# Kernel tuning notes

Hardware: AMD Instinct MI355X
Metric: run time of the kernel (lower is better)

## Reference

```python
import jax, jax.numpy as jnp
import numpy as np

B, T, C = 16, 2048, 64  # n_embd = 64


def setup_inputs() -> dict:
    key = jax.random.key(0)
    ks = jax.random.split(key, 4)
    scale = 1.0 / np.sqrt(C)
    x = jax.random.normal(ks[0], (B, T, C), dtype=jnp.float32)
    Wk = jax.random.normal(ks[1], (C, C), dtype=jnp.float32) * scale
    Wq = jax.random.normal(ks[2], (C, C), dtype=jnp.float32) * scale
    Wv = jax.random.normal(ks[3], (C, C), dtype=jnp.float32) * scale
    bk = jnp.zeros((C,), dtype=jnp.float32)
    bq = jnp.zeros((C,), dtype=jnp.float32)
    bv = jnp.zeros((C,), dtype=jnp.float32)
    return {"x": x, "Wk": Wk, "bk": bk, "Wq": Wq, "bq": bq, "Wv": Wv, "bv": bv}


def reference(x, Wk, bk, Wq, bq, Wv, bv):
    # Faithful to source: wei = q @ k^T * C**0.5 (MULTIPLY, as in original code),
    # softmax over last axis, no causal mask (tril is built but unused), dropout=0.
    _, _, c = x.shape
    k = jnp.einsum('btc,cd->btd', x, Wk) + bk
    q = jnp.einsum('btc,cd->btd', x, Wq) + bq
    v = jnp.einsum('btc,cd->btd', x, Wv) + bv
    wei = jnp.einsum('btd,bsd->bts', q, k) * (c ** 0.5)  # [B,T,T]
    wei = jax.nn.softmax(wei, axis=-1)
    out = jnp.einsum('bts,bsd->btd', wei, v)  # [B,T,C]
    return out
```

## Files before the change

### kernel.cpp

```cpp
#include <hip/hip_runtime.h>
#include <hip/hip_bf16.h>
#include <stdint.h>

#define NBATCH 16
#define NT 2048
#define NC 64
#define QT 64
#define KT 128
#define SC_LOG2E 11.5415603f

typedef __bf16 bf16x8 __attribute__((ext_vector_type(8)));
typedef _Float16 f16x8 __attribute__((ext_vector_type(8)));
typedef float f32x4 __attribute__((ext_vector_type(4)));
typedef float f32x16 __attribute__((ext_vector_type(16)));

#define Z16 {0.f,0.f,0.f,0.f,0.f,0.f,0.f,0.f,0.f,0.f,0.f,0.f,0.f,0.f,0.f,0.f}

extern "C" __device__ float __ocml_native_exp2_f32(float);
#define EXP2F(x) __ocml_native_exp2_f32(x)

static __device__ __forceinline__ unsigned short f2bf(float f) {
  __bf16 h = (__bf16)f;
  union { __bf16 h; unsigned short u; } a; a.h = h; return a.u;
}
static __device__ __forceinline__ float bf2f(unsigned short h) {
  union { uint32_t u; float f; } a; a.u = ((uint32_t)h) << 16;
  return a.f;
}
static __device__ __forceinline__ unsigned short f2h(float f) {
  _Float16 h = (_Float16)f;
  union { _Float16 h; unsigned short u; } a; a.h = h; return a.u;
}
static __device__ __forceinline__ float h2f(unsigned short u) {
  union { unsigned short u; _Float16 h; } a; a.u = u; return (float)a.h;
}
static __device__ __forceinline__ float fasu(uint32_t u) {
  union { uint32_t u; float f; } a; a.u = u; return a.f;
}
static __device__ __forceinline__ uint32_t uasf(float f) {
  union { float f; uint32_t u; } a; a.f = f; return a.u;
}
static __device__ __forceinline__ uint32_t pkh(float a, float b) {
  auto h = __builtin_amdgcn_cvt_pkrtz(a, b);
  union { decltype(h) v; uint32_t u; } c; c.v = h; return c.u;
}

#define GLD_LDS16(gsrc, ldst)                                                  \
  __builtin_amdgcn_global_load_lds(                                            \
      (const __attribute__((address_space(1))) void*)(gsrc),                   \
      (__attribute__((address_space(3))) void*)(ldst), 16, 0, 0)

__global__ __launch_bounds__(256, 2) void prep_w(
    const float* __restrict__ Wk, const float* __restrict__ Wq,
    const float* __restrict__ Wv,
    unsigned short* __restrict__ wt_hi, unsigned short* __restrict__ wt_lo)
{
  __shared__ unsigned short hbuf[64][66];
  __shared__ unsigned short lbuf[64][66];
  const int m = (int)blockIdx.x;
  const float* Wm = (m == 0) ? Wk : (m == 1 ? Wq : Wv);
  const int tid = (int)threadIdx.x;
  for (int idx = tid; idx < 1024; idx += 256) {
    int c = idx >> 4, o4 = (idx & 15) * 4;
    float4 v = *(const float4*)(Wm + c * 64 + o4);
    float vals[4] = {v.x, v.y, v.z, v.w};
#pragma unroll
    for (int j = 0; j < 4; ++j) {
      unsigned short h = f2bf(vals[j]);
      hbuf[o4 + j][c] = h;
      lbuf[o4 + j][c] = f2bf(vals[j] - bf2f(h));
    }
  }
  __syncthreads();
  for (int idx = tid; idx < 1024; idx += 256) {
    int o = idx >> 4, c0 = (idx & 15) * 4;
    ushort4 hv, lv;
    hv.x = hbuf[o][c0]; hv.y = hbuf[o][c0 + 1];
    hv.z = hbuf[o][c0 + 2]; hv.w = hbuf[o][c0 + 3];
    lv.x = lbuf[o][c0]; lv.y = lbuf[o][c0 + 1];
    lv.z = lbuf[o][c0 + 2]; lv.w = lbuf[o][c0 + 3];
    *(ushort4*)(wt_hi + (size_t)(m * 64 + o) * 64 + c0) = hv;
    *(ushort4*)(wt_lo + (size_t)(m * 64 + o) * 64 + c0) = lv;
  }
}

__global__ __launch_bounds__(256, 2) void proj_kernel(
    const float* __restrict__ x,
    const unsigned short* __restrict__ wt_hi, const unsigned short* __restrict__ wt_lo,
    const float* __restrict__ bk, const float* __restrict__ bq, const float* __restrict__ bv,
    unsigned short* __restrict__ kf, unsigned short* __restrict__ qfh,
    unsigned short* __restrict__ qfl, unsigned short* __restrict__ vt)
{
  __shared__ __align__(16) char smem[65536];
  const int XH = 0, XL = 8192, WTH = 16384, WTL = 40960, VTB = 0;
  const int tid = (int)threadIdx.x;
  const int l = tid & 63, w = tid >> 6;
  const int lr = l & 15, lg = l >> 4;
  const int blk = (int)blockIdx.x;
  const int rowbase = blk * 64;
  const int bb = blk >> 5;

  float4 xv[4];
#pragma unroll
  for (int j = 0; j < 4; ++j) {
    int c = tid + j * 256;
    int row = c >> 4, d0 = (c & 15) * 4;
    xv[j] = *(const float4*)(x + (size_t)(rowbase + row) * NC + d0);
  }
#pragma unroll
  for (int ch4 = 0; ch4 < 6; ++ch4) {
    int ch = ch4 * 4 + w;
    int d = ch * 1024 + l * 16;
    int swk = d ^ (((d >> 7) & 7) << 4);
    GLD_LDS16((const char*)wt_hi + swk, smem + WTH + ch * 1024);
    GLD_LDS16((const char*)wt_lo + swk, smem + WTL + ch * 1024);
  }
#pragma unroll
  for (int j = 0; j < 4; ++j) {
    int c = tid + j * 256;
    int row = c >> 4, d0 = (c & 15) * 4;
    unsigned short h0 = f2bf(xv[j].x), h1 = f2bf(xv[j].y), h2 = f2bf(xv[j].z), h3 = f2bf(xv[j].w);
    unsigned short m0 = f2bf(xv[j].x - bf2f(h0)), m1 = f2bf(xv[j].y - bf2f(h1));
    unsigned short m2 = f2bf(xv[j].z - bf2f(h2)), m3 = f2bf(xv[j].w - bf2f(h3));
    uint2 ph, pl;
    ph.x = (uint32_t)h0 | ((uint32_t)h1 << 16); ph.y = (uint32_t)h2 | ((uint32_t)h3 << 16);
    pl.x = (uint32_t)m0 | ((uint32_t)m1 << 16); pl.y = (uint32_t)m2 | ((uint32_t)m3 << 16);
    int byteoff = (row * 128 + d0 * 2) ^ ((row & 7) << 4);
    *(uint2*)(smem + XH + byteoff) = ph;
    *(uint2*)(smem + XL + byteoff) = pl;
  }
  __syncthreads();

  bf16x8 xh[2], xl[2];
  {
    int row = w * 16 + lr;
#pragma unroll
    for (int dc = 0; dc < 2; ++dc) {
      int byteoff = (row * 128 + (dc * 32 + lg * 8) * 2) ^ ((row & 7) << 4);
      xh[dc] = *(const bf16x8*)(smem + XH + byteoff);
      xl[dc] = *(const bf16x8*)(smem + XL + byteoff);
    }
  }
  f32x4 acc[12];
#pragma unroll
  for (int nb = 0; nb < 12; ++nb) {
    f32x4 a = {0.f, 0.f, 0.f, 0.f};
    int og = nb * 16 + lr;
#pragma unroll
    for (int dc = 0; dc < 2; ++dc) {
      int byteoff = (og * 128 + (dc * 32 + lg * 8) * 2) ^ ((og & 7) << 4);
      bf16x8 bh = *(const bf16x8*)(smem + WTH + byteoff);
      bf16x8 bl = *(const bf16x8*)(smem + WTL + byteoff);
      a = __builtin_amdgcn_mfma_f32_16x16x32_bf16(bh, xh[dc], a, 0, 0, 0);
      a = __builtin_amdgcn_mfma_f32_16x16x32_bf16(bl, xh[dc], a, 0, 0, 0);
      a = __builtin_amdgcn_mfma_f32_16x16x32_bf16(bh, xl[dc], a, 0, 0, 0);
    }
    acc[nb] = a;
  }
  __syncthreads();

  const int tloc = w * 16 + lr;
  const size_t gt = (size_t)(rowbase + tloc);
#pragma unroll
  for (int nb = 0; nb < 12; ++nb) {
    int ogb = (nb & 3) * 16 + lg * 4;
    const float* bp = (nb < 4) ? bk : (nb < 8 ? bq : bv);
    float4 bias = *(const float4*)(bp + ogb);
    float v0 = acc[nb][0] + bias.x, v1 = acc[nb][1] + bias.y,
          v2 = acc[nb][2] + bias.z, v3 = acc[nb][3] + bias.w;
    if (nb < 4) {
      ushort4 hv;
      hv.x = f2h(v0); hv.y = f2h(v1); hv.z = f2h(v2); hv.w = f2h(v3);
      *(ushort4*)(kf + gt * 64 + ogb) = hv;
    } else if (nb < 8) {
      v0 *= SC_LOG2E; v1 *= SC_LOG2E; v2 *= SC_LOG2E; v3 *= SC_LOG2E;
      ushort4 hv, lv;
      hv.x = f2h(v0); lv.x = f2h(v0 - h2f(hv.x));
      hv.y = f2h(v1); lv.y = f2h(v1 - h2f(hv.y));
      hv.z = f2h(v2); lv.z = f2h(v2 - h2f(hv.z));
      hv.w = f2h(v3); lv.w = f2h(v3 - h2f(hv.w));
      *(ushort4*)(qfh + gt * 64 + ogb) = hv;
      *(ushort4*)(qfl + gt * 64 + ogb) = lv;
    } else {
      float vs[4] = {v0, v1, v2, v3};
#pragma unroll
      for (int r = 0; r < 4; ++r) {
        int o = ogb + r;
        int byteoff = (o * 128 + tloc * 2) ^ ((o & 7) << 4);
        *(unsigned short*)(smem + VTB + byteoff) = f2h(vs[r]);
      }
    }
  }
  __syncthreads();
  for (int cc = tid; cc < 512; cc += 256) {
    int o = cc >> 3, t0 = (cc & 7) * 8;
    int byteoff = (o * 128 + t0 * 2) ^ ((o & 7) << 4);
    uint4 v = *(const uint4*)(smem + VTB + byteoff);
    *(uint4*)(vt + ((size_t)bb * 64 + o) * NT + (size_t)(blk & 31) * 64 + t0) = v;
  }
}

__global__ __launch_bounds__(512, 4) void attn_kernel(
    const unsigned short* __restrict__ kf, const unsigned short* __restrict__ qfh,
    const unsigned short* __restrict__ qfl, const unsigned short* __restrict__ vt,
    float* __restrict__ out)
{
  __shared__ __align__(16) char smem[65536];
  const int KB_A = 0, KB_B = 16384;
  const int VB_0 = 32768, VB_1 = 49152;
  const int MLB = 49152;
  const int tid = (int)threadIdx.x;
  const int l = tid & 63, w = tid >> 6;
  const int lq = l & 31;
  const bool hi = (l >= 32);
  const int hioff = hi ? 16 : 0;
  const int r = w & 1;
  const int cc = w >> 1;
  const int lb = ((int)(blockIdx.x & 7) << 6) | ((int)blockIdx.x >> 3);
  const int bb = lb >> 5;
  const int qt = lb & 31;

  const char* k_base = (const char*)(kf + (size_t)bb * NT * 64);
  const char* v_base = (const char*)(vt + (size_t)bb * 64 * NT);

#define STAGE_TILE(kb_, vb_, it_)                                              \
  do {                                                                         \
    const char* k_t = k_base + (size_t)(it_) * 16384;                          \
    const char* v_tb = v_base + (size_t)(it_) * 256;                           \
    _Pragma("unroll")                                                          \
    for (int j = 0; j < 2; ++j) {                                              \
      int ch = 2 * w + j;                                                      \
      int d = ch * 1024 + l * 16;                                              \
      int swk = d ^ (((d >> 7) & 7) << 4);                                     \
      GLD_LDS16(k_t + swk, smem + (kb_) + ch * 1024);                          \
      int o = d >> 8;                                                          \
      int swv = (d & 255) ^ ((o & 7) << 4);                                    \
      GLD_LDS16(v_tb + (size_t)o * 4096 + swv, smem + (vb_) + ch * 1024);      \
    }                                                                          \
  } while (0)

  STAGE_TILE(KB_A, VB_0, 0);
  f16x8 Qh[4], Ql[4];
  {
    const char* qh_t = (const char*)qfh + ((size_t)bb * NT + (size_t)qt * QT) * 128;
    const char* ql_t = (const char*)qfl + ((size_t)bb * NT + (size_t)qt * QT) * 128;
    int qrow = r * 32 + lq;
#pragma unroll
    for (int dc = 0; dc < 4; ++dc) {
      Qh[dc] = *(const f16x8*)(qh_t + qrow * 128 + dc * 32 + hioff);
      Ql[dc] = *(const f16x8*)(ql_t + qrow * 128 + dc * 32 + hioff);
    }
  }
  asm volatile("s_waitcnt vmcnt(0)" ::: "memory");
  __builtin_amdgcn_s_barrier();
  asm volatile("" ::: "memory");

  f32x16 O0 = Z16, O1 = Z16;
  float mrun = -1e30f, lrun = 0.f;
  const int swr = (lq & 7) << 4;

  for (int it = 0; it < NT / KT; ++it) {
    const int cbk = (it & 1) ? KB_B : KB_A;
    const int cbv = (it & 1) ? VB_1 : VB_0;
    if (it + 1 < NT / KT)
      STAGE_TILE((it & 1) ? KB_A : KB_B, (it & 1) ? VB_0 : VB_1, it + 1);

    f32x16 S = Z16;
    __builtin_amdgcn_s_setprio(1);
#pragma unroll
    for (int dc = 0; dc < 4; ++dc) {
      int krow = cc * 32 + lq;
      int cchunk = (dc * 32 + hioff) ^ swr;
      f16x8 Kf = *(const f16x8*)(smem + cbk + krow * 128 + cchunk);
      S = __builtin_amdgcn_mfma_f32_32x32x16_f16(Kf, Qh[dc], S, 0, 0, 0);
      S = __builtin_amdgcn_mfma_f32_32x32x16_f16(Kf, Ql[dc], S, 0, 0, 0);
    }
    __builtin_amdgcn_s_setprio(0);

    float a01 = fmaxf(S[0], S[1]),   a23 = fmaxf(S[2], S[3]);
    float a45 = fmaxf(S[4], S[5]),   a67 = fmaxf(S[6], S[7]);
    float a89 = fmaxf(S[8], S[9]),   aab = fmaxf(S[10], S[11]);
    float acd = fmaxf(S[12], S[13]), aef = fmaxf(S[14], S[15]);
    float pmax = fmaxf(fmaxf(fmaxf(a01, a23), fmaxf(a45, a67)),
                       fmaxf(fmaxf(a89, aab), fmaxf(acd, aef)));
    {
      auto sw = __builtin_amdgcn_permlane32_swap(uasf(pmax), uasf(pmax), false, false);
      pmax = fmaxf(fasu(sw[0]), fasu(sw[1]));
    }
    if (__any(pmax > mrun + 11.55f)) {
      float mnew = fmaxf(mrun, pmax);
      float alpha = EXP2F(mrun - mnew);
      O0 *= alpha; O1 *= alpha; lrun *= alpha; mrun = mnew;
    }
    float p[16];
    float ts = 0.f;
#pragma unroll
    for (int i = 0; i < 16; ++i) { p[i] = EXP2F(S[i] - mrun); ts += p[i]; }
    {
      auto sw = __builtin_amdgcn_permlane32_swap(uasf(ts), uasf(ts), false, false);
      ts = fasu(sw[0]) + fasu(sw[1]);
    }
    lrun += ts;

    __builtin_amdgcn_s_setprio(1);
#pragma unroll
    for (int kc = 0; kc < 2; ++kc) {
      const int b_ = 8 * kc;
      uint32_t X0 = pkh(p[b_+0], p[b_+1]);
      uint32_t X1 = pkh(p[b_+2], p[b_+3]);
      uint32_t Y0 = pkh(p[b_+4], p[b_+5]);
      uint32_t Y1 = pkh(p[b_+6], p[b_+7]);
      auto sw0 = __builtin_amdgcn_permlane32_swap(X0, Y0, false, false);
      auto sw1 = __builtin_amdgcn_permlane32_swap(X1, Y1, false, false);
      union { uint32_t u[4]; f16x8 v; } cvb;
      cvb.u[0] = sw0[0]; cvb.u[1] = sw1[0];
      cvb.u[2] = sw0[1]; cvb.u[3] = sw1[1];
      int vcol = 64 * cc + 32 * kc + hioff;
      f16x8 Av0 = *(const f16x8*)(smem + cbv + lq * 256 + (vcol ^ swr));
      f16x8 Av1 = *(const f16x8*)(smem + cbv + (32 + lq) * 256 + (vcol ^ swr));
      O0 = __builtin_amdgcn_mfma_f32_32x32x16_f16(Av0, cvb.v, O0, 0, 0, 0);
      O1 = __builtin_amdgcn_mfma_f32_32x32x16_f16(Av1, cvb.v, O1, 0, 0, 0);
    }
    __builtin_amdgcn_s_setprio(0);

    asm volatile("s_waitcnt vmcnt(0)" ::: "memory");
    __builtin_amdgcn_s_barrier();
    asm volatile("" ::: "memory");
    __builtin_amdgcn_sched_barrier(0);
  }

  const int lsw = (l & 7) << 4;
#define DUMP(idx_)                                                             \
  {                                                                            \
    char* dd = smem + (idx_) * 8192 + l * 128;                                 \
    _Pragma("unroll")                                                          \
    for (int g = 0; g < 4; ++g) {                                              \
      f32x4 t0, t1;                                                            \
      _Pragma("unroll")                                                        \
      for (int j = 0; j < 4; ++j) { t0[j] = O0[4*g+j]; t1[j] = O1[4*g+j]; }    \
      *(f32x4*)(dd + ((g * 16) ^ lsw)) = t0;                                   \
      *(f32x4*)(dd + ((64 + g * 16) ^ lsw)) = t1;                              \
    }                                                                          \
    *(float*)(smem + MLB + (idx_) * 256 + lq * 8) = mrun;                      \
    *(float*)(smem + MLB + (idx_) * 256 + lq * 8 + 4) = lrun;                  \
  }
#define MERGE(idx_)                                                            \
  {                                                                            \
    const char* ds = smem + (idx_) * 8192 + l * 128;                           \
    float m1 = *(const float*)(smem + MLB + (idx_) * 256 + lq * 8);            \
    float l1 = *(const float*)(smem + MLB + (idx_) * 256 + lq * 8 + 4);        \
    float M = fmaxf(mrun, m1);                                                 \
    float a0 = EXP2F(mrun - M);                                                \
    float a1 = EXP2F(m1 - M);                                                  \
    lrun = lrun * a0 + l1 * a1;                                                \
    mrun = M;                                                                  \
    _Pragma("unroll")                                                          \
    for (int g = 0; g < 4; ++g) {                                              \
      f32x4 o1a = *(const f32x4*)(ds + ((g * 16) ^ lsw));                      \
      f32x4 o1b = *(const f32x4*)(ds + ((64 + g * 16) ^ lsw));                 \
      _Pragma("unroll")                                                        \
      for (int j = 0; j < 4; ++j) {                                            \
        O0[4*g+j] = O0[4*g+j] * a0 + o1a[j] * a1;                              \
        O1[4*g+j] = O1[4*g+j] * a0 + o1b[j] * a1;                              \
      }                                                                        \
    }                                                                          \
  }
  if (cc & 1) DUMP(r * 2 + (cc >> 1));
  __syncthreads();
  if (!(cc & 1)) MERGE(r * 2 + (cc >> 1));
  __syncthreads();
  if (cc == 2) DUMP(r * 2 + 1);
  __syncthreads();
  if (cc == 0) {
    MERGE(r * 2 + 1);
    float inv = 1.0f / lrun;
    float* orow = out + ((size_t)bb * NT + (size_t)qt * QT + r * 32 + lq) * 64;
#pragma unroll
    for (int g = 0; g < 4; ++g) {
      int d0 = 8 * g + (hi ? 4 : 0);
      f32x4 s0, s1;
#pragma unroll
      for (int j = 0; j < 4; ++j) { s0[j] = O0[4*g+j] * inv; s1[j] = O1[4*g+j] * inv; }
      *(f32x4*)(orow + d0) = s0;
      *(f32x4*)(orow + d0 + 32) = s1;
    }
  }
#undef DUMP
#undef MERGE
#undef STAGE_TILE
}

extern "C" void kernel_launch(void* const* d_in, const int* in_sizes, int n_in,
                              void* d_out, int out_size, void* d_ws, size_t ws_size,
                              hipStream_t stream) {
  const float* x  = (const float*)d_in[0];
  const float* Wk = (const float*)d_in[1];
  const float* bk = (const float*)d_in[2];
  const float* Wq = (const float*)d_in[3];
  const float* bq = (const float*)d_in[4];
  const float* Wv = (const float*)d_in[5];
  const float* bv = (const float*)d_in[6];
  float* out = (float*)d_out;

  const size_t NE = (size_t)NBATCH * NT * 64;
  unsigned short* ws = (unsigned short*)d_ws;
  unsigned short* kf  = ws;
  unsigned short* qfh = ws + NE;
  unsigned short* qfl = ws + 2 * NE;
  unsigned short* vt  = ws + 3 * NE;
  unsigned short* wt_hi = ws + 4 * NE;
  unsigned short* wt_lo = wt_hi + 192 * 64;

  prep_w<<<dim3(3), dim3(256), 0, stream>>>(Wk, Wq, Wv, wt_hi, wt_lo);
  proj_kernel<<<dim3((NBATCH * NT) / 64), dim3(256), 0, stream>>>(
      x, wt_hi, wt_lo, bk, bq, bv, kf, qfh, qfl, vt);
  attn_kernel<<<dim3(NBATCH * (NT / QT)), dim3(512), 0, stream>>>(
      kf, qfh, qfl, vt, out);
}
```

Baseline: 61.54 us.

## Software-pipeline QK^T of next tile with softmax/PV of previous tile

Restructures the attention loop so that each iteration computes the QK^T scores for the current key tile while running softmax and the PV MFMA for the previous tile's scores. A third V buffer is added and LDS grows to 80 KB, with two tiles prefetched before the loop and buffer indices rotated each step. The aim is to overlap MFMA work with the exp/max VALU work and hide latency. In exchange, higher LDS use per block can reduce occupancy, and a barrier is added before the final merge.

Result: slower. 64.46 us (+4.7%).

```diff
diff --git a/kernel.cpp b/kernel.cpp
--- a/kernel.cpp
+++ b/kernel.cpp
@@ -205,9 +205,9 @@
     const unsigned short* __restrict__ qfl, const unsigned short* __restrict__ vt,
     float* __restrict__ out)
 {
-  __shared__ __align__(16) char smem[65536];
+  __shared__ __align__(16) char smem[81920];
   const int KB_A = 0, KB_B = 16384;
-  const int VB_0 = 32768, VB_1 = 49152;
+  const int VB_0 = 32768, VB_1 = 49152, VB_2 = 65536;
   const int MLB = 49152;
   const int tid = (int)threadIdx.x;
   const int l = tid & 63, w = tid >> 6;
@@ -240,6 +240,7 @@
   } while (0)
 
   STAGE_TILE(KB_A, VB_0, 0);
+  STAGE_TILE(KB_B, VB_1, 1);
   f16x8 Qh[4], Ql[4];
   {
     const char* qh_t = (const char*)qfh + ((size_t)bb * NT + (size_t)qt * QT) * 128;
@@ -259,75 +260,101 @@
   float mrun = -1e30f, lrun = 0.f;
   const int swr = (lq & 7) << 4;
 
-  for (int it = 0; it < NT / KT; ++it) {
-    const int cbk = (it & 1) ? KB_B : KB_A;
-    const int cbv = (it & 1) ? VB_1 : VB_0;
-    if (it + 1 < NT / KT)
-      STAGE_TILE((it & 1) ? KB_A : KB_B, (it & 1) ? VB_0 : VB_1, it + 1);
-
-    f32x16 S = Z16;
-    __builtin_amdgcn_s_setprio(1);
-#pragma unroll
-    for (int dc = 0; dc < 4; ++dc) {
-      int krow = cc * 32 + lq;
-      int cchunk = (dc * 32 + hioff) ^ swr;
-      f16x8 Kf = *(const f16x8*)(smem + cbk + krow * 128 + cchunk);
-      S = __builtin_amdgcn_mfma_f32_32x32x16_f16(Kf, Qh[dc], S, 0, 0, 0);
-      S = __builtin_amdgcn_mfma_f32_32x32x16_f16(Kf, Ql[dc], S, 0, 0, 0);
-    }
-    __builtin_amdgcn_s_setprio(0);
-
-    float a01 = fmaxf(S[0], S[1]),   a23 = fmaxf(S[2], S[3]);
-    float a45 = fmaxf(S[4], S[5]),   a67 = fmaxf(S[6], S[7]);
-    float a89 = fmaxf(S[8], S[9]),   aab = fmaxf(S[10], S[11]);
-    float acd = fmaxf(S[12], S[13]), aef = fmaxf(S[14], S[15]);
-    float pmax = fmaxf(fmaxf(fmaxf(a01, a23), fmaxf(a45, a67)),
-                       fmaxf(fmaxf(a89, aab), fmaxf(acd, aef)));
-    {
-      auto sw = __builtin_amdgcn_permlane32_swap(uasf(pmax), uasf(pmax), false, false);
-      pmax = fmaxf(fasu(sw[0]), fasu(sw[1]));
-    }
-    if (__any(pmax > mrun + 11.55f)) {
-      float mnew = fmaxf(mrun, pmax);
-      float alpha = EXP2F(mrun - mnew);
-      O0 *= alpha; O1 *= alpha; lrun *= alpha; mrun = mnew;
-    }
-    float p[16];
-    float ts = 0.f;
-#pragma unroll
-    for (int i = 0; i < 16; ++i) { p[i] = EXP2F(S[i] - mrun); ts += p[i]; }
-    {
-      auto sw = __builtin_amdgcn_permlane32_swap(uasf(ts), uasf(ts), false, false);
-      ts = fasu(sw[0]) + fasu(sw[1]);
-    }
-    lrun += ts;
-
-    __builtin_amdgcn_s_setprio(1);
-#pragma unroll
-    for (int kc = 0; kc < 2; ++kc) {
-      const int b_ = 8 * kc;
-      uint32_t X0 = pkh(p[b_+0], p[b_+1]);
-      uint32_t X1 = pkh(p[b_+2], p[b_+3]);
-      uint32_t Y0 = pkh(p[b_+4], p[b_+5]);
-      uint32_t Y1 = pkh(p[b_+6], p[b_+7]);
-      auto sw0 = __builtin_amdgcn_permlane32_swap(X0, Y0, false, false);
-      auto sw1 = __builtin_amdgcn_permlane32_swap(X1, Y1, false, false);
-      union { uint32_t u[4]; f16x8 v; } cvb;
-      cvb.u[0] = sw0[0]; cvb.u[1] = sw1[0];
-      cvb.u[2] = sw0[1]; cvb.u[3] = sw1[1];
-      int vcol = 64 * cc + 32 * kc + hioff;
-      f16x8 Av0 = *(const f16x8*)(smem + cbv + lq * 256 + (vcol ^ swr));
-      f16x8 Av1 = *(const f16x8*)(smem + cbv + (32 + lq) * 256 + (vcol ^ swr));
-      O0 = __builtin_amdgcn_mfma_f32_32x32x16_f16(Av0, cvb.v, O0, 0, 0, 0);
-      O1 = __builtin_amdgcn_mfma_f32_32x32x16_f16(Av1, cvb.v, O1, 0, 0, 0);
-    }
-    __builtin_amdgcn_s_setprio(0);
-
-    asm volatile("s_waitcnt vmcnt(0)" ::: "memory");
-    __builtin_amdgcn_s_barrier();
-    asm volatile("" ::: "memory");
-    __builtin_amdgcn_sched_barrier(0);
-  }
+#define QK_TILE(kb_, SC_)                                                      \
+  {                                                                            \
+    int krow_ = cc * 32 + lq;                                                  \
+    __builtin_amdgcn_s_setprio(1);                                             \
+    _Pragma("unroll")                                                          \
+    for (int dc = 0; dc < 4; ++dc) {                                           \
+      int cchunk_ = (dc * 32 + hioff) ^ swr;                                   \
+      f16x8 Kf_ = *(const f16x8*)(smem + (kb_) + krow_ * 128 + cchunk_);       \
+      SC_ = __builtin_amdgcn_mfma_f32_32x32x16_f16(Kf_, Qh[dc], SC_, 0, 0, 0); \
+      SC_ = __builtin_amdgcn_mfma_f32_32x32x16_f16(Kf_, Ql[dc], SC_, 0, 0, 0); \
+    }                                                                          \
+    __builtin_amdgcn_s_setprio(0);                                             \
+  }
+
+#define SMPV(SP_, vb_)                                                         \
+  {                                                                            \
+    float a01 = fmaxf(SP_[0], SP_[1]),   a23 = fmaxf(SP_[2], SP_[3]);          \
+    float a45 = fmaxf(SP_[4], SP_[5]),   a67 = fmaxf(SP_[6], SP_[7]);          \
+    float a89 = fmaxf(SP_[8], SP_[9]),   aab = fmaxf(SP_[10], SP_[11]);        \
+    float acd = fmaxf(SP_[12], SP_[13]), aef = fmaxf(SP_[14], SP_[15]);        \
+    float pmax = fmaxf(fmaxf(fmaxf(a01, a23), fmaxf(a45, a67)),                \
+                       fmaxf(fmaxf(a89, aab), fmaxf(acd, aef)));               \
+    {                                                                          \
+      auto sw_ = __builtin_amdgcn_permlane32_swap(uasf(pmax), uasf(pmax), false, false); \
+      pmax = fmaxf(fasu(sw_[0]), fasu(sw_[1]));                                \
+    }                                                                          \
+    if (__any(pmax > mrun + 11.55f)) {                                         \
+      float mnew = fmaxf(mrun, pmax);                                          \
+      float alpha = EXP2F(mrun - mnew);                                        \
+      O0 *= alpha; O1 *= alpha; lrun *= alpha; mrun = mnew;                    \
+    }                                                                          \
+    float p[16];                                                               \
+    float ts = 0.f;                                                            \
+    _Pragma("unroll")                                                          \
+    for (int i = 0; i < 16; ++i) { p[i] = EXP2F(SP_[i] - mrun); ts += p[i]; }  \
+    {                                                                          \
+      auto sw_ = __builtin_amdgcn_permlane32_swap(uasf(ts), uasf(ts), false, false); \
+      ts = fasu(sw_[0]) + fasu(sw_[1]);                                        \
+    }                                                                          \
+    lrun += ts;                                                                \
+    __builtin_amdgcn_s_setprio(1);                                             \
+    _Pragma("unroll")                                                          \
+    for (int kc = 0; kc < 2; ++kc) {                                           \
+      const int b_ = 8 * kc;                                                   \
+      uint32_t X0 = pkh(p[b_+0], p[b_+1]);                                     \
+      uint32_t X1 = pkh(p[b_+2], p[b_+3]);                                     \
+      uint32_t Y0 = pkh(p[b_+4], p[b_+5]);                                     \
+      uint32_t Y1 = pkh(p[b_+6], p[b_+7]);                                     \
+      auto sw0_ = __builtin_amdgcn_permlane32_swap(X0, Y0, false, false);      \
+      auto sw1_ = __builtin_amdgcn_permlane32_swap(X1, Y1, false, false);      \
+      union { uint32_t u[4]; f16x8 v; } cvb_;                                  \
+      cvb_.u[0] = sw0_[0]; cvb_.u[1] = sw1_[0];                                \
+      cvb_.u[2] = sw0_[1]; cvb_.u[3] = sw1_[1];                                \
+      int vcol_ = 64 * cc + 32 * kc + hioff;                                   \
+      f16x8 Av0_ = *(const f16x8*)(smem + (vb_) + lq * 256 + (vcol_ ^ swr));   \
+      f16x8 Av1_ = *(const f16x8*)(smem + (vb_) + (32 + lq) * 256 + (vcol_ ^ swr)); \
+      O0 = __builtin_amdgcn_mfma_f32_32x32x16_f16(Av0_, cvb_.v, O0, 0, 0, 0);  \
+      O1 = __builtin_amdgcn_mfma_f32_32x32x16_f16(Av1_, cvb_.v, O1, 0, 0, 0);  \
+    }                                                                          \
+    __builtin_amdgcn_s_setprio(0);                                             \
+  }
+
+  f32x16 SA = Z16, SB = Z16;
+  QK_TILE(KB_A, SA);
+  asm volatile("s_waitcnt lgkmcnt(0)" ::: "memory");
+  __builtin_amdgcn_s_barrier();
+  asm volatile("" ::: "memory");
+
+  int kbC = KB_B, kbN = KB_A;
+  int vbP = VB_0, vbC = VB_1, vbN = VB_2;
+
+#define BODY(i_, SP_, SC_, STG_)                                               \
+  {                                                                            \
+    if (STG_) STAGE_TILE(kbN, vbN, (i_) + 1);                                  \
+    SC_ = Z16;                                                                 \
+    QK_TILE(kbC, SC_);                                                         \
+    SMPV(SP_, vbP);                                                            \
+    asm volatile("s_waitcnt vmcnt(0)" ::: "memory");                           \
+    __builtin_amdgcn_s_barrier();                                              \
+    asm volatile("" ::: "memory");                                             \
+    __builtin_amdgcn_sched_barrier(0);                                         \
+  }
+#define ROT()                                                                  \
+  { int t_ = vbP; vbP = vbC; vbC = vbN; vbN = t_;                              \
+    t_ = kbC; kbC = kbN; kbN = t_; }
+
+#pragma unroll 1
+  for (int ib = 0; ib < 7; ++ib) {
+    BODY(2 * ib + 1, SA, SB, 1)
+    ROT()
+    BODY(2 * ib + 2, SB, SA, 1)
+    ROT()
+  }
+  BODY(15, SA, SB, 0)
+  SMPV(SB, vbC);
 
   const int lsw = (l & 7) << 4;
 #define DUMP(idx_)                                                             \
@@ -365,6 +392,7 @@
       }                                                                        \
     }                                                                          \
   }
+  __syncthreads();
   if (cc & 1) DUMP(r * 2 + (cc >> 1));
   __syncthreads();
   if (!(cc & 1)) MERGE(r * 2 + (cc >> 1));
@@ -387,6 +415,10 @@
   }
 #undef DUMP
 #undef MERGE
+#undef BODY
+#undef ROT
+#undef SMPV
+#undef QK_TILE
 #undef STAGE_TILE
 }
 
```
